# Kernel tuning notes

Measured on AMD Instinct MI355X. Metric: run time of the kernel, lower is better.

## Reference

```python
import jax, jax.numpy as jnp
from jax import lax
import numpy as np
from math import lgamma

N_MELS = 80; MEMORY_DIM = 512; PRENET = (256, 256)
ATTN_LSTM = 1024; ATTN_DIM = 128
N_STATIC = 8; SF = 21; N_DYN = 8; DF = 21
PRIOR_LEN = 11; ALPHA = 0.1; BETA = 0.9
DEC_LSTM = 1024; R = 2
B = 32; T_MELS = 800; T_ENC = 200


def _betabinom_pmf(k, n, a, b):
    lbeta = lambda x, y: lgamma(x) + lgamma(y) - lgamma(x + y)
    return np.exp(lgamma(n + 1) - lgamma(k + 1) - lgamma(n - k + 1) + lbeta(k + a, n - k + b) - lbeta(a, b))


def setup_inputs() -> dict:
    key = jax.random.key(0)
    ks = iter(jax.random.split(key, 40))
    w = lambda shape, s=0.05: jax.random.normal(next(ks), shape, jnp.float32) * s
    # prior filter, flipped as in the torch buffer (so cross-correlation == convolution with pmf)
    prior = np.array([_betabinom_pmf(k, PRIOR_LEN - 1, ALPHA, BETA) for k in range(PRIOR_LEN)], np.float32)[::-1].copy()
    return {
        "mels": w((B, N_MELS, T_MELS), 1.0),
        "memory": w((B, T_ENC, MEMORY_DIM), 1.0),
        "prenet_W1": w((PRENET[0], N_MELS)), "prenet_b1": jnp.zeros((PRENET[0],), jnp.float32),
        "prenet_W2": w((PRENET[1], PRENET[0])), "prenet_b2": jnp.zeros((PRENET[1],), jnp.float32),
        "attn_Wih": w((4 * ATTN_LSTM, PRENET[1] + MEMORY_DIM)), "attn_Whh": w((4 * ATTN_LSTM, ATTN_LSTM)),
        "attn_bih": jnp.zeros((4 * ATTN_LSTM,), jnp.float32), "attn_bhh": jnp.zeros((4 * ATTN_LSTM,), jnp.float32),
        "dca_Wq": w((ATTN_DIM, ATTN_LSTM)), "dca_bq": jnp.zeros((ATTN_DIM,), jnp.float32),
        "dca_V": w((N_DYN * DF, ATTN_DIM)),
        "dca_F": w((N_STATIC, 1, SF)),
        "dca_U": w((ATTN_DIM, N_STATIC)),
        "dca_T": w((ATTN_DIM, N_DYN)), "dca_Tb": jnp.zeros((ATTN_DIM,), jnp.float32),
        "dca_v": w((1, ATTN_DIM)),
        "prior": jnp.asarray(prior),
        "dec_Wih": w((4 * DEC_LSTM, ATTN_LSTM + MEMORY_DIM)), "dec_Whh": w((4 * DEC_LSTM, DEC_LSTM)),
        "dec_bih": jnp.zeros((4 * DEC_LSTM,), jnp.float32), "dec_bhh": jnp.zeros((4 * DEC_LSTM,), jnp.float32),
        "ac_W": w((N_MELS * R, DEC_LSTM + MEMORY_DIM)), "ac_b": jnp.zeros((N_MELS * R,), jnp.float32),
    }


def _lstm_cell(x, h, c, Wih, Whh, bih, bhh):
    g = x @ Wih.T + bih + h @ Whh.T + bhh
    i, f, gg, o = jnp.split(g, 4, axis=-1)  # torch gate order i,f,g,o
    c_new = jax.nn.sigmoid(f) * c + jax.nn.sigmoid(i) * jnp.tanh(gg)
    h_new = jax.nn.sigmoid(o) * jnp.tanh(c_new)
    return h_new, c_new


def _conv1d(x, k, pad, groups=1):
    # x: [B, Cin, T], k: [Cout, Cin/groups, K]; cross-correlation, like torch conv1d
    return lax.conv_general_dilated(x, k, (1,), [pad], feature_group_count=groups)


def _dca_step(query, memory, aw, prior, Wq, bq, V, Fk, U, Tw, Tb, v):
    Bsz, T = aw.shape
    # location prior: causal conv with (flipped) betabinom pmf
    p = _conv1d(aw[:, None, :], prior[None, None, :], (PRIOR_LEN - 1, 0))[:, 0, :]
    p = jnp.log(jnp.maximum(p, 1e-6))
    # dynamic filters predicted from query, applied per-batch via grouped conv
    G = jnp.tanh(query @ Wq.T + bq) @ V.T  # [B, N_DYN*DF]
    g = _conv1d(aw[None, :, :], G.reshape(Bsz * N_DYN, 1, DF), ((DF - 1) // 2, (DF - 1) // 2), groups=Bsz)
    g = g.reshape(Bsz, N_DYN, T).transpose(0, 2, 1)  # [B, T, N_DYN]
    # static location filters
    f = _conv1d(aw[:, None, :], Fk, ((SF - 1) // 2, (SF - 1) // 2)).transpose(0, 2, 1)  # [B, T, N_STATIC]
    e = (jnp.tanh(f @ U.T + g @ Tw.T + Tb) @ v.T)[:, :, 0] + p  # [B, T]
    aw_new = jax.nn.softmax(e, axis=-1)
    ctx = jnp.einsum("bt,btd->bd", aw_new, memory)
    return aw_new, ctx


def reference(mels, memory, prenet_W1, prenet_b1, prenet_W2, prenet_b2, attn_Wih, attn_Whh, attn_bih, attn_bhh, dca_Wq, dca_bq, dca_V, dca_F, dca_U, dca_T, dca_Tb, dca_v, prior, dec_Wih, dec_Whh, dec_bih, dec_bhh, ac_W, ac_b):
    Bsz, n_mels, T_mels = mels.shape
    T_enc = memory.shape[1]
    n_steps = T_mels // R
    go = jnp.zeros((Bsz, n_mels), mels.dtype)
    # teacher forcing: step t>0 consumes ground-truth frame at index t*R - 1
    tf = mels[:, :, R - 1::R][:, :, : n_steps - 1].transpose(2, 0, 1)
    frames = jnp.concatenate([go[None], tf], axis=0)  # [S, B, n_mels]
    aw0 = jnp.zeros((Bsz, T_enc), mels.dtype).at[:, 0].set(1.0)  # one-hot init attention
    carry0 = (jnp.zeros((Bsz, MEMORY_DIM), mels.dtype),
              jnp.zeros((Bsz, ATTN_LSTM), mels.dtype), jnp.zeros((Bsz, ATTN_LSTM), mels.dtype),
              jnp.zeros((Bsz, DEC_LSTM), mels.dtype), jnp.zeros((Bsz, DEC_LSTM), mels.dtype),
              aw0)

    def step(carry, frame):
        ctx, ah, acs, dh, dcs, aw = carry
        x = jax.nn.relu(frame @ prenet_W1.T + prenet_b1)
        x = jax.nn.relu(x @ prenet_W2.T + prenet_b2)
        ah, acs = _lstm_cell(jnp.concatenate([ctx, x], -1), ah, acs, attn_Wih, attn_Whh, attn_bih, attn_bhh)
        aw, ctx = _dca_step(ah, memory, aw, prior, dca_Wq, dca_bq, dca_V, dca_F, dca_U, dca_T, dca_Tb, dca_v)
        dh, dcs = _lstm_cell(jnp.concatenate([ah, ctx], -1), dh, dcs, dec_Wih, dec_Whh, dec_bih, dec_bhh)
        out = jnp.concatenate([dh, ctx], -1) @ ac_W.T + ac_b  # [B, n_mels*R]
        return (ctx, ah, acs, dh, dcs, aw), (out, aw)

    _, (outs, aws) = lax.scan(step, carry0, frames)
    # per-step [B, n_mels, R] frames concatenated along time (step-major)
    output_mels = outs.reshape(n_steps, Bsz, n_mels, R).transpose(1, 2, 0, 3).reshape(Bsz, n_mels, n_steps * R)
    alignments = aws.transpose(1, 2, 0)  # [B, T_enc, n_steps]
    return output_mels, alignments
```

## Files before the change

kernel.cpp:

```cpp
#include <hip/hip_runtime.h>
#include <hip/hip_bf16.h>

typedef unsigned short u16;
typedef unsigned int   u32;
typedef float f32x4 __attribute__((ext_vector_type(4)));

#define NTHR 256
#define NBLK 512
#define NGRP 64
#define GRPSZ 8
#define ROOT (NBLK - 1)

#define BATCH 32
#define TENC  200
#define NMELS 80
#define TMELS 800
#define NSTEP 400

#define BAR_CNT(g)  ((g)*32)
#define BAR_FLAG(g) (2048 + (g)*32)
#define BAR_GEN     4096

#define OFF_AHC   0
#define OFF_ACS   65536
#define OFF_DHC   98304
#define OFF_DCS   163840
#define OFF_CTX   196608
#define OFF_AW    229376
#define OFF_FBUF  236544
#define OFF_PBUF  287744
#define OFF_GPC   294912
#define OFF_X     425984
#define FLOAT_END 3702784
#define ZERO_CNT  236544

#define B_AWIH 0
#define B_AWHH 3145728
#define B_DWIH 7340032
#define B_DWHH 13631488
#define B_ACW  17825792
#define B_WQ   18071552
#define B_MEMT 18202624

#define NTLD4(dst, src) \
  asm volatile("global_load_dwordx4 %0, %1, off sc0 sc1" : "=v"(dst) : "v"(src))
#define NTLD1(dst, src) \
  asm volatile("global_load_dword %0, %1, off sc0 sc1" : "=v"(dst) : "v"(src))
#define NTFENCE() do { \
  asm volatile("s_waitcnt vmcnt(0)" ::: "memory"); \
  __builtin_amdgcn_sched_barrier(0); } while (0)

struct KArgs {
  const float *mels, *memory, *pW1, *pb1, *pW2, *pb2;
  const float *aWih, *aWhh, *abih, *abhh;
  const float *Wq, *bq, *V, *F, *U, *T, *Tb, *vv, *prior;
  const float *dWih, *dWhh, *dbih, *dbhh, *acW, *acb;
  float *out;
  float *ws;
  u16   *wb;
  int   *bar;
};

__device__ __forceinline__ float sigf(float x) {
  x = fminf(fmaxf(x, -30.f), 30.f);
  return 1.0f / (1.0f + __expf(-x));
}
__device__ __forceinline__ float ftanh(float x) {
  x = fminf(fmaxf(x, -15.f), 15.f);
  float e = __expf(2.f * x);
  return (e - 1.f) / (e + 1.f);
}
__device__ __forceinline__ float blo(u32 u) {
  union { u32 i; float f; } v; v.i = u << 16; return v.f;
}
__device__ __forceinline__ float bhi(u32 u) {
  union { u32 i; float f; } v; v.i = u & 0xffff0000u; return v.f;
}
__device__ __forceinline__ u16 f2b(float x) {
  __hip_bfloat16 h = __float2bfloat16(x);
  return *reinterpret_cast<u16*>(&h);
}

__device__ __forceinline__ void gbar(int* bar, int* s_bail, int& gen) {
  const int tid = threadIdx.x;
  const int bid = blockIdx.x;
  const int t = ++gen;
  __syncthreads();
  if (!*s_bail) {
    if (tid == 0) {
      int a_ = __hip_atomic_fetch_add(&bar[BAR_CNT(bid >> 3)], 1,
                                      __ATOMIC_RELEASE, __HIP_MEMORY_SCOPE_AGENT);
      if (a_ == GRPSZ - 1) {
        __hip_atomic_store(&bar[BAR_CNT(bid >> 3)], 0, __ATOMIC_RELAXED, __HIP_MEMORY_SCOPE_AGENT);
        __hip_atomic_store(&bar[BAR_FLAG(bid >> 3)], t, __ATOMIC_RELEASE, __HIP_MEMORY_SCOPE_AGENT);
      }
    }
    if (bid == ROOT) {
      if (tid < NGRP) {
        int it = 0;
        while (__hip_atomic_load(&bar[BAR_FLAG(tid)], __ATOMIC_RELAXED, __HIP_MEMORY_SCOPE_AGENT) < t) {
          __builtin_amdgcn_s_sleep(1);
          if (++it > (1 << 24)) { *s_bail = 1; break; }
        }
      }
      __syncthreads();
      if (tid == 0)
        __hip_atomic_store(&bar[BAR_GEN], t, __ATOMIC_RELEASE, __HIP_MEMORY_SCOPE_AGENT);
    } else if (tid == 0) {
      int it = 0;
      while (__hip_atomic_load(&bar[BAR_GEN], __ATOMIC_RELAXED, __HIP_MEMORY_SCOPE_AGENT) < t) {
        __builtin_amdgcn_s_sleep(1);
        if (++it > (1 << 24)) { *s_bail = 1; break; }
      }
    }
  }
  __syncthreads();
}

__device__ __forceinline__ float dotK(const float* xs, const u16* w, int K) {
  const uint4* wp = (const uint4*)w;
  const float4* xp = (const float4*)xs;
  float a0 = 0.f, a1 = 0.f, a2 = 0.f, a3 = 0.f;
  #pragma unroll 2
  for (int i = 0; i < (K >> 5); ++i) {
    uint4 w0 = wp[i*4+0], w1 = wp[i*4+1], w2 = wp[i*4+2], w3 = wp[i*4+3];
    float4 x0 = xp[i*8+0], x1 = xp[i*8+1], x2 = xp[i*8+2], x3 = xp[i*8+3];
    float4 x4 = xp[i*8+4], x5 = xp[i*8+5], x6 = xp[i*8+6], x7 = xp[i*8+7];
    a0 += blo(w0.x)*x0.x + bhi(w0.x)*x0.y + blo(w0.y)*x0.z + bhi(w0.y)*x0.w
        + blo(w0.z)*x1.x + bhi(w0.z)*x1.y + blo(w0.w)*x1.z + bhi(w0.w)*x1.w;
    a1 += blo(w1.x)*x2.x + bhi(w1.x)*x2.y + blo(w1.y)*x2.z + bhi(w1.y)*x2.w
        + blo(w1.z)*x3.x + bhi(w1.z)*x3.y + blo(w1.w)*x3.z + bhi(w1.w)*x3.w;
    a2 += blo(w2.x)*x4.x + bhi(w2.x)*x4.y + blo(w2.y)*x4.z + bhi(w2.y)*x4.w
        + blo(w2.z)*x5.x + bhi(w2.z)*x5.y + blo(w2.w)*x5.z + bhi(w2.w)*x5.w;
    a3 += blo(w3.x)*x6.x + bhi(w3.x)*x6.y + blo(w3.y)*x6.z + bhi(w3.y)*x6.w
        + blo(w3.z)*x7.x + bhi(w3.z)*x7.y + blo(w3.w)*x7.z + bhi(w3.w)*x7.w;
  }
  return (a0 + a1) + (a2 + a3);
}

__device__ __forceinline__ void j1_job(const KArgs& a, float* sm, int s) {
  const int tid = threadIdx.x, bid = blockIdx.x;
  const int ug = bid & 63, bg = bid >> 6;
  float* ws = a.ws;
  const u16* wb = a.wb;
  const int pprev = (s + 1) & 1, pcur = s & 1;
  const float* ctxp = ws + OFF_CTX + pprev * 16384;
  const float* ahp  = ws + OFF_AHC + pprev * 32768;
  const float* Xs   = ws + OFF_X + s * 8192;
  float* xbuf = sm;
  float* sred = sm + 8224;
  {
    const int bq = tid >> 6, lane = tid & 63;
    const int b = bg*4 + bq;
    const float* ctxb = ctxp + b*512;
    const float* Xb   = Xs + b*256;
    auto ap = [&](int idx) -> const f32x4* {
      if (idx < 128) return (const f32x4*)(ctxb + idx*4);
      if (idx < 192) return (const f32x4*)(Xb + (idx-128)*4);
      const int u = (idx-192)*4;
      return (const f32x4*)(ahp + (bg*64 + (u>>4))*64 + bq*16 + (u&15));
    };
    f32x4 v0,v1,v2,v3,v4,v5,v6;
    NTLD4(v0, ap(lane));       NTLD4(v1, ap(lane+64));
    NTLD4(v2, ap(lane+128));   NTLD4(v3, ap(lane+192));
    NTLD4(v4, ap(lane+256));   NTLD4(v5, ap(lane+320));
    NTLD4(v6, ap(lane+384));
    NTFENCE();
    f32x4* dst = (f32x4*)(xbuf + bq*1800);
    dst[lane] = v0; dst[lane+64] = v1; dst[lane+128] = v2; dst[lane+192] = v3;
    dst[lane+256] = v4; dst[lane+320] = v5; dst[lane+384] = v6;
  }
  __syncthreads();
  {
    const int r8 = tid >> 2, bsub = tid & 3;
    const int gate = r8 >> 4, ui = r8 & 15;
    const int rr = gate*1024 + ug*16 + ui;
    const float* xs = xbuf + bsub*1800;
    float acc = dotK(xs, wb + B_AWIH + rr*768, 768)
              + dotK(xs + 768, wb + B_AWHH + rr*1024, 1024)
              + a.abih[rr] + a.abhh[rr];
    sred[tid] = acc;
  }
  __syncthreads();
  if (tid < 64) {
    const int ui2 = tid >> 2, b2 = tid & 3;
    const float gi = sred[(ui2)*4 + b2];
    const float gf = sred[(16+ui2)*4 + b2];
    const float gg = sred[(32+ui2)*4 + b2];
    const float go = sred[(48+ui2)*4 + b2];
    float* acs = ws + OFF_ACS;
    const float c = sigf(gf)*acs[bid*64 + tid] + sigf(gi)*ftanh(gg);
    acs[bid*64 + tid] = c;
    (ws + OFF_AHC + pcur*32768)[bid*64 + b2*16 + ui2] = sigf(go)*ftanh(c);
  }
}

__device__ __forceinline__ void jg_job(const KArgs& a, float* sm, int s, int j) {
  const int tid = threadIdx.x;
  const int ug = j & 63, bg = j >> 6;
  float* ws = a.ws;
  const u16* wb = a.wb;
  const float* dhp = ws + OFF_DHC + ((s+1)&1)*32768;
  const float* ahp = ws + OFF_AHC + (s&1)*32768;
  float* xbuf = sm;
  __syncthreads();
  {
    const int bq = tid >> 6, lane = tid & 63;
    auto ap = [&](int idx) -> const f32x4* {
      if (idx < 256) { const int u = idx*4;
        return (const f32x4*)(dhp + (bg*64 + (u>>4))*64 + bq*16 + (u&15)); }
      const int u = (idx-256)*4;
      return (const f32x4*)(ahp + (bg*64 + (u>>4))*64 + bq*16 + (u&15));
    };
    f32x4 v0,v1,v2,v3,v4,v5,v6,v7;
    NTLD4(v0, ap(lane));       NTLD4(v1, ap(lane+64));
    NTLD4(v2, ap(lane+128));   NTLD4(v3, ap(lane+192));
    NTLD4(v4, ap(lane+256));   NTLD4(v5, ap(lane+320));
    NTLD4(v6, ap(lane+384));   NTLD4(v7, ap(lane+448));
    NTFENCE();
    f32x4* dst = (f32x4*)(xbuf + bq*2056);
    dst[lane] = v0; dst[lane+64] = v1; dst[lane+128] = v2; dst[lane+192] = v3;
    dst[lane+256] = v4; dst[lane+320] = v5; dst[lane+384] = v6; dst[lane+448] = v7;
  }
  __syncthreads();
  {
    const int r8 = tid >> 2, bsub = tid & 3;
    const int gate = r8 >> 4, ui = r8 & 15;
    const int rr = gate*1024 + ug*16 + ui;
    const float* xs = xbuf + bsub*2056;
    float acc = dotK(xs, wb + B_DWHH + rr*1024, 1024)
              + dotK(xs + 1024, wb + B_DWIH + rr*1536, 1024)
              + a.dbih[rr] + a.dbhh[rr];
    (ws + OFF_GPC)[j*256 + tid] = acc;
  }
}

__device__ __forceinline__ void p3_job(const KArgs& a, float* sm, int s) {
  const int tid = threadIdx.x, bid = blockIdx.x;
  const int ug = bid & 63, bg = bid >> 6;
  float* ws = a.ws;
  const u16* wb = a.wb;
  const float* ctxc = ws + OFF_CTX + (s&1)*16384;
  float* xbuf = sm;
  float* sred = sm + 8224;
  __syncthreads();
  const int bq = tid >> 6, lane = tid & 63;
  const int b = bg*4 + bq;
  f32x4 v0, v1; float gp;
  NTLD4(v0, (const f32x4*)(ctxc + b*512 + lane*4));
  NTLD4(v1, (const f32x4*)(ctxc + b*512 + (lane+64)*4));
  NTLD1(gp, (ws + OFF_GPC + bid*256 + tid));
  NTFENCE();
  ((f32x4*)(xbuf + bq*520))[lane] = v0;
  ((f32x4*)(xbuf + bq*520))[lane+64] = v1;
  __syncthreads();
  {
    const int r8 = tid >> 2, bsub = tid & 3;
    const int gate = r8 >> 4, ui = r8 & 15;
    const int rr = gate*1024 + ug*16 + ui;
    (void)gate; (void)ui;
    float acc = dotK(xbuf + bsub*520, wb + B_DWIH + rr*1536 + 1024, 512) + gp;
    sred[tid] = acc;
  }
  __syncthreads();
  if (tid < 64) {
    const int ui2 = tid >> 2, b2 = tid & 3;
    const float gi = sred[(ui2)*4 + b2];
    const float gf = sred[(16+ui2)*4 + b2];
    const float gg = sred[(32+ui2)*4 + b2];
    const float go = sred[(48+ui2)*4 + b2];
    float* dcs = ws + OFF_DCS;
    const float c = sigf(gf)*dcs[bid*64 + tid] + sigf(gi)*ftanh(gg);
    dcs[bid*64 + tid] = c;
    (ws + OFF_DHC + (s&1)*32768)[bid*64 + b2*16 + ui2] = sigf(go)*ftanh(c);
  }
}

__device__ __forceinline__ void j4_job(const KArgs& a, float* sm) {
  const int tid = threadIdx.x, b4 = blockIdx.x;
  float* ws = a.ws;
  float* aw   = ws + OFF_AW;
  float* fbuf = ws + OFF_FBUF;
  float* pbuf = ws + OFF_PBUF;
  __syncthreads();
  if (tid < 224) sm[tid] = (tid >= 10 && tid < 210) ? aw[b4*224 + tid - 10] : 0.f;
  __syncthreads();
  if (tid < 200) {
    #pragma unroll
    for (int j = 0; j < 8; ++j) {
      float p = 0.f;
      #pragma unroll
      for (int tau = 0; tau < 21; ++tau) p += sm[tid + tau] * a.F[j*21 + tau];
      fbuf[b4*1600 + tid*8 + j] = p;
    }
    float pp = 0.f;
    #pragma unroll
    for (int tau = 0; tau < 11; ++tau) pp += sm[tid + tau] * a.prior[tau];
    pbuf[b4*224 + tid] = __logf(fmaxf(pp, 1e-6f));
  }
}

__device__ __forceinline__ void outproj_job(const KArgs& a, float* sm, int sprev) {
  const int tid = threadIdx.x, bid = blockIdx.x;
  const int og = bid - 192, rg = og >> 3, bg = og & 7;
  const int pdm = sprev & 1;
  float* ws = a.ws;
  const u16* wb = a.wb;
  const float* dhp  = ws + OFF_DHC + pdm*32768;
  const float* ctxp = ws + OFF_CTX + pdm*16384;
  float* xbuf = sm;
  float* sred = sm + 8224;
  __syncthreads();
  {
    const int bq = tid >> 6, lane = tid & 63;
    const int b = bg*4 + bq;
    auto ap = [&](int idx) -> const f32x4* {
      if (idx < 256) { const int u = idx*4;
        return (const f32x4*)(dhp + (bg*64 + (u>>4))*64 + bq*16 + (u&15)); }
      return (const f32x4*)(ctxp + b*512 + (idx-256)*4);
    };
    f32x4 v0,v1,v2,v3,v4,v5;
    NTLD4(v0, ap(lane));       NTLD4(v1, ap(lane+64));
    NTLD4(v2, ap(lane+128));   NTLD4(v3, ap(lane+192));
    NTLD4(v4, ap(lane+256));   NTLD4(v5, ap(lane+320));
    NTFENCE();
    f32x4* dst = (f32x4*)(xbuf + bq*1544);
    dst[lane] = v0; dst[lane+64] = v1; dst[lane+128] = v2; dst[lane+192] = v3;
    dst[lane+256] = v4; dst[lane+320] = v5;
  }
  __syncthreads();
  {
    const int kc = tid & 7, r = (tid >> 3) & 7, bq = tid >> 6;
    const int rr = rg*8 + r;
    float p = dotK(xbuf + bq*1544 + kc*192, wb + B_ACW + rr*1536 + kc*192, 192);
    sred[tid] = p;
  }
  __syncthreads();
  if (tid < 32) {
    const int bq2 = tid >> 3, r2 = tid & 7;
    const int rr2 = rg*8 + r2, b2 = bg*4 + bq2;
    float tot = a.acb[rr2];
    #pragma unroll
    for (int q = 0; q < 8; ++q) tot += sred[bq2*64 + r2*8 + q];
    a.out[(b2*NMELS + (rr2 >> 1))*TMELS + sprev*2 + (rr2 & 1)] = tot;
  }
}

__device__ __forceinline__ void dca_step(const KArgs& a, float* sm, int s) {
  const int tid = threadIdx.x, b = blockIdx.x;
  const u16* wb = a.wb;
  float* ws = a.ws;
  const int pc = s & 1;
  const float* ahp = ws + OFF_AHC + pc*32768;
  float* ctx  = ws + OFF_CTX + pc*16384;
  float* aw   = ws + OFF_AW;
  const float* fbuf = ws + OFF_FBUF;
  const float* pbuf = ws + OFF_PBUF;
  float* s_ah  = sm;
  float* s_awp = sm + 1024;
  float* s_q   = sm + 1248;
  float* s_G   = sm + 1376;
  float* s_e   = sm + 1552;
  float* s_gg  = sm + 1760;
  float* s_ff  = sm + 3360;
  float* s_red = sm + 4960;
  float* s_awn = sm + 5216;
  f32x4 vah;
  {
    const int u = tid*4;
    NTLD4(vah, (const f32x4*)(ahp + ((b>>2)*64 + (u>>4))*64 + (b&3)*16 + (u&15)));
  }
  if (tid < 224) s_awp[tid] = (tid >= 10 && tid < 210) ? aw[b*224 + tid - 10] : 0.f;
  for (int i = tid; i < 1600; i += NTHR) s_ff[i] = fbuf[b*1600 + i];
  NTFENCE();
  *(f32x4*)(s_ah + tid*4) = vah;
  __syncthreads();
  {
    const int o = tid & 127, half = tid >> 7;
    const uint4* wq = (const uint4*)(wb + B_WQ + o*1024 + half*512);
    const float* xa = s_ah + half*512;
    float p = 0.f;
    #pragma unroll 8
    for (int q8 = 0; q8 < 64; ++q8) {
      uint4 w = wq[q8];
      const float* xq = xa + q8*8;
      p += blo(w.x)*xq[0] + bhi(w.x)*xq[1] + blo(w.y)*xq[2] + bhi(w.y)*xq[3]
         + blo(w.z)*xq[4] + bhi(w.z)*xq[5] + blo(w.w)*xq[6] + bhi(w.w)*xq[7];
    }
    s_red[tid] = p;
  }
  __syncthreads();
  if (tid < 128) s_q[tid] = ftanh(s_red[tid] + s_red[128 + tid] + a.bq[tid]);
  __syncthreads();
  if (tid < 168) {
    const float4* vp = (const float4*)(a.V + tid*128);
    float p = 0.f;
    #pragma unroll
    for (int q4 = 0; q4 < 32; ++q4) {
      float4 w = vp[q4];
      const float* xq = s_q + q4*4;
      p += w.x*xq[0] + w.y*xq[1] + w.z*xq[2] + w.w*xq[3];
    }
    s_G[tid] = p;
  }
  __syncthreads();
  for (int idx = tid; idx < 1600; idx += NTHR) {
    const int pos = idx >> 3, d = idx & 7;
    float p = 0.f;
    #pragma unroll
    for (int tau = 0; tau < 21; ++tau) p += s_awp[pos + tau] * s_G[d*21 + tau];
    s_gg[idx] = p;
  }
  __syncthreads();
  #pragma unroll 1
  for (int ro = 0; ro < 4; ++ro) {
    const int pos = ro*64 + (tid >> 2), sub = tid & 3;
    float av = 0.f;
    if (pos < 200) {
      const float* fpos = s_ff + pos*8;
      const float* gpos = s_gg + pos*8;
      #pragma unroll 4
      for (int fi = 0; fi < 32; ++fi) {
        const int ff = sub*32 + fi;
        const float4* Up = (const float4*)(a.U + ff*8);
        const float4* Tp = (const float4*)(a.T + ff*8);
        float4 u0 = Up[0], u1 = Up[1], t0 = Tp[0], t1 = Tp[1];
        float h = a.Tb[ff];
        h += u0.x*fpos[0] + u0.y*fpos[1] + u0.z*fpos[2] + u0.w*fpos[3]
           + u1.x*fpos[4] + u1.y*fpos[5] + u1.z*fpos[6] + u1.w*fpos[7];
        h += t0.x*gpos[0] + t0.y*gpos[1] + t0.z*gpos[2] + t0.w*gpos[3]
           + t1.x*gpos[4] + t1.y*gpos[5] + t1.z*gpos[6] + t1.w*gpos[7];
        av += a.vv[ff] * ftanh(h);
      }
    }
    av += __shfl_xor(av, 1);
    av += __shfl_xor(av, 2);
    if (sub == 0 && pos < 200) s_e[pos] = av + pbuf[b*224 + pos];
  }
  __syncthreads();
  float mval = (tid < 200) ? s_e[tid] : -1e30f;
  #pragma unroll
  for (int off = 32; off > 0; off >>= 1) mval = fmaxf(mval, __shfl_xor(mval, off));
  if ((tid & 63) == 0) s_red[tid >> 6] = mval;
  __syncthreads();
  const float m = fmaxf(fmaxf(s_red[0], s_red[1]), fmaxf(s_red[2], s_red[3]));
  const float ex = (tid < 200) ? __expf(s_e[tid] - m) : 0.f;
  float sv = ex;
  #pragma unroll
  for (int off = 32; off > 0; off >>= 1) sv += __shfl_xor(sv, off);
  if ((tid & 63) == 0) s_red[4 + (tid >> 6)] = sv;
  __syncthreads();
  const float inv = 1.f / (s_red[4] + s_red[5] + s_red[6] + s_red[7]);
  if (tid < 200) {
    const float awv = ex * inv;
    aw[b*224 + tid] = awv;
    s_awn[tid] = awv;
    a.out[2048000 + b*80000 + tid*400 + s] = awv;
  }
  __syncthreads();
  #pragma unroll 1
  for (int d = tid; d < 512; d += NTHR) {
    const uint4* mp = (const uint4*)(wb + B_MEMT + b*102400 + d*200);
    float p = 0.f;
    #pragma unroll 5
    for (int q = 0; q < 25; ++q) {
      uint4 v = mp[q];
      const float* aa = s_awn + q*8;
      p += blo(v.x)*aa[0] + bhi(v.x)*aa[1] + blo(v.y)*aa[2] + bhi(v.y)*aa[3]
         + blo(v.z)*aa[4] + bhi(v.z)*aa[5] + blo(v.w)*aa[6] + bhi(v.w)*aa[7];
    }
    ctx[b*512 + d] = p;
  }
}

__global__ __launch_bounds__(NTHR) void init_kernel(KArgs a) {
  const int gtid = blockIdx.x*NTHR + threadIdx.x;
  const int str = gridDim.x*NTHR;
  float* ws = a.ws;
  for (int i = gtid; i < 8192; i += str) a.bar[i] = 0;
  for (int i = gtid; i < ZERO_CNT; i += str) ws[i] = 0.f;
  float* aw = ws + OFF_AW;
  for (int i = gtid; i < 32*224; i += str) aw[i] = ((i % 224) == 0) ? 1.f : 0.f;
}

__global__ __launch_bounds__(NTHR) void conv_kernel(KArgs a) {
  const int gtid = blockIdx.x*NTHR + threadIdx.x;
  const int str = gridDim.x*NTHR;
  u16* wb = a.wb;
  for (int i = gtid; i < 3145728; i += str) wb[B_AWIH + i] = f2b(a.aWih[i]);
  for (int i = gtid; i < 4194304; i += str) wb[B_AWHH + i] = f2b(a.aWhh[i]);
  for (int i = gtid; i < 6291456; i += str) wb[B_DWIH + i] = f2b(a.dWih[i]);
  for (int i = gtid; i < 4194304; i += str) wb[B_DWHH + i] = f2b(a.dWhh[i]);
  for (int i = gtid; i < 245760;  i += str) wb[B_ACW  + i] = f2b(a.acW[i]);
  for (int i = gtid; i < 131072;  i += str) wb[B_WQ   + i] = f2b(a.Wq[i]);
  for (int i = gtid; i < 3276800; i += str) {
    const int b = i / 102400, rem = i - b*102400;
    const int d = rem / 200, t = rem - d*200;
    wb[B_MEMT + i] = f2b(a.memory[b*102400 + t*512 + d]);
  }
}

__global__ __launch_bounds__(NTHR) void prenet_kernel(KArgs a) {
  __shared__ float sm[384];
  const int tid = threadIdx.x;
  const int pair = blockIdx.x;
  const int s = pair >> 5, b = pair & 31;
  float* X = a.ws + OFF_X;
  if (tid < 80) {
    float v = 0.f;
    if (s > 0) v = a.mels[(b*NMELS + tid)*TMELS + 2*s - 1];
    sm[tid] = v;
  }
  __syncthreads();
  float a1 = a.pb1[tid];
  #pragma unroll 4
  for (int k = 0; k < 80; ++k) a1 += a.pW1[tid*80 + k] * sm[k];
  a1 = fmaxf(a1, 0.f);
  __syncthreads();
  sm[128 + tid] = a1;
  __syncthreads();
  float a2 = a.pb2[tid];
  #pragma unroll 4
  for (int k = 0; k < 256; ++k) a2 += a.pW2[tid*256 + k] * sm[128 + k];
  a2 = fmaxf(a2, 0.f);
  X[(s*BATCH + b)*256 + tid] = a2;
}

__global__ __launch_bounds__(NTHR, 2) void loop_kernel(KArgs a) {
  __shared__ float sm[8480];
  __shared__ int s_bail;
  const int tid = threadIdx.x;
  const int bid = blockIdx.x;
  int* bar = a.bar;
  int gen = 0;
  if (tid == 0) s_bail = 0;
  __syncthreads();

  j1_job(a, sm, 0);
  if (bid < 32) j4_job(a, sm);
  gbar(bar, &s_bail, gen);

  for (int s = 0; s < NSTEP; ++s) {
    if (bid < 32) {
      dca_step(a, sm, s);
    } else {
      jg_job(a, sm, s, bid - 32);
      if (bid < 64) jg_job(a, sm, s, bid + 448);
    }
    gbar(bar, &s_bail, gen);
    if (s + 1 < NSTEP) j1_job(a, sm, s + 1);
    p3_job(a, sm, s);
    if (bid < 32 && s + 1 < NSTEP) j4_job(a, sm);
    if (bid >= 192 && bid < 352 && s > 0) outproj_job(a, sm, s - 1);
    gbar(bar, &s_bail, gen);
  }

  if (bid >= 192 && bid < 352) outproj_job(a, sm, NSTEP - 1);
}

extern "C" void kernel_launch(void* const* d_in, const int* in_sizes, int n_in,
                              void* d_out, int out_size, void* d_ws, size_t ws_size,
                              hipStream_t stream) {
  (void)in_sizes; (void)n_in; (void)out_size; (void)ws_size;
  KArgs a;
  a.mels   = (const float*)d_in[0];
  a.memory = (const float*)d_in[1];
  a.pW1 = (const float*)d_in[2];  a.pb1 = (const float*)d_in[3];
  a.pW2 = (const float*)d_in[4];  a.pb2 = (const float*)d_in[5];
  a.aWih = (const float*)d_in[6]; a.aWhh = (const float*)d_in[7];
  a.abih = (const float*)d_in[8]; a.abhh = (const float*)d_in[9];
  a.Wq = (const float*)d_in[10];  a.bq = (const float*)d_in[11];
  a.V  = (const float*)d_in[12];  a.F  = (const float*)d_in[13];
  a.U  = (const float*)d_in[14];  a.T  = (const float*)d_in[15];
  a.Tb = (const float*)d_in[16];  a.vv = (const float*)d_in[17];
  a.prior = (const float*)d_in[18];
  a.dWih = (const float*)d_in[19]; a.dWhh = (const float*)d_in[20];
  a.dbih = (const float*)d_in[21]; a.dbhh = (const float*)d_in[22];
  a.acW  = (const float*)d_in[23]; a.acb  = (const float*)d_in[24];
  a.out = (float*)d_out;
  a.bar = (int*)d_ws;
  a.ws  = (float*)((char*)d_ws + 32768);
  a.wb  = (u16*)(a.ws + FLOAT_END);

  hipLaunchKernelGGL(init_kernel, dim3(512), dim3(NTHR), 0, stream, a);
  hipLaunchKernelGGL(conv_kernel, dim3(2048), dim3(NTHR), 0, stream, a);
  hipLaunchKernelGGL(prenet_kernel, dim3(NSTEP*BATCH), dim3(NTHR), 0, stream, a);
  hipLaunchKernelGGL(loop_kernel, dim3(NBLK), dim3(NTHR), 0, stream, a);
}
```

Before: 58.78 ms.

## Remap block-to-unit assignment, move outproj to first phase, use fast reciprocal

Remaps which unit group and batch group each block handles and adds a matching chunked layout (chunkW) for the hidden-state buffers. The output projection moves out of the second barrier phase into the first, running on blocks 64-223 alongside jg_job and the DCA step, which shortens the critical second phase. The prenet input X now uses a plain cached load. Divisions in sigmoid, tanh and softmax become hardware reciprocal approximations, and the outproj shared-memory staging is padded to reduce bank conflicts. The reciprocal approximation trades a small amount of accuracy for speed, and the new block mapping changes the data locality pattern.

```diff
diff --git a/kernel.cpp b/kernel.cpp
--- a/kernel.cpp
+++ b/kernel.cpp
@@ -61,14 +61,15 @@
   int   *bar;
 };
 
+__device__ __forceinline__ float frcp(float x) { return __builtin_amdgcn_rcpf(x); }
 __device__ __forceinline__ float sigf(float x) {
   x = fminf(fmaxf(x, -30.f), 30.f);
-  return 1.0f / (1.0f + __expf(-x));
+  return frcp(1.0f + __expf(-x));
 }
 __device__ __forceinline__ float ftanh(float x) {
   x = fminf(fmaxf(x, -15.f), 15.f);
   float e = __expf(2.f * x);
-  return (e - 1.f) / (e + 1.f);
+  return (e - 1.f) * frcp(e + 1.f);
 }
 __device__ __forceinline__ float blo(u32 u) {
   union { u32 i; float f; } v; v.i = u << 16; return v.f;
@@ -79,6 +80,9 @@
 __device__ __forceinline__ u16 f2b(float x) {
   __hip_bfloat16 h = __float2bfloat16(x);
   return *reinterpret_cast<u16*>(&h);
+}
+__device__ __forceinline__ int chunkW(int ug_, int bg_) {
+  return ((ug_ >> 3) + 8*bg_ + 64*(ug_ & 7)) * 64;
 }
 
 __device__ __forceinline__ void gbar(int* bar, int* s_bail, int& gen) {
@@ -140,7 +144,7 @@
 
 __device__ __forceinline__ void j1_job(const KArgs& a, float* sm, int s) {
   const int tid = threadIdx.x, bid = blockIdx.x;
-  const int ug = bid & 63, bg = bid >> 6;
+  const int ug = (bid & 7)*8 + (bid >> 6), bg = (bid >> 3) & 7;
   float* ws = a.ws;
   const u16* wb = a.wb;
   const int pprev = (s + 1) & 1, pcur = s & 1;
@@ -153,18 +157,16 @@
     const int bq = tid >> 6, lane = tid & 63;
     const int b = bg*4 + bq;
     const float* ctxb = ctxp + b*512;
-    const float* Xb   = Xs + b*256;
-    auto ap = [&](int idx) -> const f32x4* {
-      if (idx < 128) return (const f32x4*)(ctxb + idx*4);
-      if (idx < 192) return (const f32x4*)(Xb + (idx-128)*4);
-      const int u = (idx-192)*4;
-      return (const f32x4*)(ahp + (bg*64 + (u>>4))*64 + bq*16 + (u&15));
+    auto ah_at = [&](int idx) -> const f32x4* {
+      const int u = (idx - 192)*4;
+      return (const f32x4*)(ahp + chunkW(u >> 4, bg) + bq*16 + (u & 15));
     };
-    f32x4 v0,v1,v2,v3,v4,v5,v6;
-    NTLD4(v0, ap(lane));       NTLD4(v1, ap(lane+64));
-    NTLD4(v2, ap(lane+128));   NTLD4(v3, ap(lane+192));
-    NTLD4(v4, ap(lane+256));   NTLD4(v5, ap(lane+320));
-    NTLD4(v6, ap(lane+384));
+    f32x4 v0,v1,v3,v4,v5,v6;
+    NTLD4(v0, (const f32x4*)(ctxb + lane*4));
+    NTLD4(v1, (const f32x4*)(ctxb + (lane+64)*4));
+    NTLD4(v3, ah_at(lane+192)); NTLD4(v4, ah_at(lane+256));
+    NTLD4(v5, ah_at(lane+320)); NTLD4(v6, ah_at(lane+384));
+    f32x4 v2 = *((const f32x4*)(Xs + b*256 + lane*4));
     NTFENCE();
     f32x4* dst = (f32x4*)(xbuf + bq*1800);
     dst[lane] = v0; dst[lane+64] = v1; dst[lane+128] = v2; dst[lane+192] = v3;
@@ -197,7 +199,7 @@
 
 __device__ __forceinline__ void jg_job(const KArgs& a, float* sm, int s, int j) {
   const int tid = threadIdx.x;
-  const int ug = j & 63, bg = j >> 6;
+  const int ug = (j & 7)*8 + (j >> 6), bg = (j >> 3) & 7;
   float* ws = a.ws;
   const u16* wb = a.wb;
   const float* dhp = ws + OFF_DHC + ((s+1)&1)*32768;
@@ -208,9 +210,9 @@
     const int bq = tid >> 6, lane = tid & 63;
     auto ap = [&](int idx) -> const f32x4* {
       if (idx < 256) { const int u = idx*4;
-        return (const f32x4*)(dhp + (bg*64 + (u>>4))*64 + bq*16 + (u&15)); }
+        return (const f32x4*)(dhp + chunkW(u >> 4, bg) + bq*16 + (u & 15)); }
       const int u = (idx-256)*4;
-      return (const f32x4*)(ahp + (bg*64 + (u>>4))*64 + bq*16 + (u&15));
+      return (const f32x4*)(ahp + chunkW(u >> 4, bg) + bq*16 + (u & 15));
     };
     f32x4 v0,v1,v2,v3,v4,v5,v6,v7;
     NTLD4(v0, ap(lane));       NTLD4(v1, ap(lane+64));
@@ -237,7 +239,7 @@
 
 __device__ __forceinline__ void p3_job(const KArgs& a, float* sm, int s) {
   const int tid = threadIdx.x, bid = blockIdx.x;
-  const int ug = bid & 63, bg = bid >> 6;
+  const int ug = (bid & 7)*8 + (bid >> 6), bg = (bid >> 3) & 7;
   float* ws = a.ws;
   const u16* wb = a.wb;
   const float* ctxc = ws + OFF_CTX + (s&1)*16384;
@@ -258,7 +260,6 @@
     const int r8 = tid >> 2, bsub = tid & 3;
     const int gate = r8 >> 4, ui = r8 & 15;
     const int rr = gate*1024 + ug*16 + ui;
-    (void)gate; (void)ui;
     float acc = dotK(xbuf + bsub*520, wb + B_DWIH + rr*1536 + 1024, 512) + gp;
     sred[tid] = acc;
   }
@@ -302,7 +303,7 @@
 
 __device__ __forceinline__ void outproj_job(const KArgs& a, float* sm, int sprev) {
   const int tid = threadIdx.x, bid = blockIdx.x;
-  const int og = bid - 192, rg = og >> 3, bg = og & 7;
+  const int og = bid - 64, rg = og >> 3, bg = og & 7;
   const int pdm = sprev & 1;
   float* ws = a.ws;
   const u16* wb = a.wb;
@@ -316,7 +317,7 @@
     const int b = bg*4 + bq;
     auto ap = [&](int idx) -> const f32x4* {
       if (idx < 256) { const int u = idx*4;
-        return (const f32x4*)(dhp + (bg*64 + (u>>4))*64 + bq*16 + (u&15)); }
+        return (const f32x4*)(dhp + chunkW(u >> 4, bg) + bq*16 + (u & 15)); }
       return (const f32x4*)(ctxp + b*512 + (idx-256)*4);
     };
     f32x4 v0,v1,v2,v3,v4,v5;
@@ -324,15 +325,19 @@
     NTLD4(v2, ap(lane+128));   NTLD4(v3, ap(lane+192));
     NTLD4(v4, ap(lane+256));   NTLD4(v5, ap(lane+320));
     NTFENCE();
-    f32x4* dst = (f32x4*)(xbuf + bq*1544);
-    dst[lane] = v0; dst[lane+64] = v1; dst[lane+128] = v2; dst[lane+192] = v3;
-    dst[lane+256] = v4; dst[lane+320] = v5;
+    float* base = xbuf + bq*1600;
+    auto put = [&](int f, f32x4 v) {
+      const int cf = f / 48, wf = f % 48;
+      *(f32x4*)(base + cf*200 + wf*4) = v;
+    };
+    put(lane, v0); put(lane+64, v1); put(lane+128, v2);
+    put(lane+192, v3); put(lane+256, v4); put(lane+320, v5);
   }
   __syncthreads();
   {
     const int kc = tid & 7, r = (tid >> 3) & 7, bq = tid >> 6;
     const int rr = rg*8 + r;
-    float p = dotK(xbuf + bq*1544 + kc*192, wb + B_ACW + rr*1536 + kc*192, 192);
+    float p = dotK(xbuf + bq*1600 + kc*200, wb + B_ACW + rr*1536 + kc*192, 192);
     sred[tid] = p;
   }
   __syncthreads();
@@ -368,7 +373,7 @@
   f32x4 vah;
   {
     const int u = tid*4;
-    NTLD4(vah, (const f32x4*)(ahp + ((b>>2)*64 + (u>>4))*64 + (b&3)*16 + (u&15)));
+    NTLD4(vah, (const f32x4*)(ahp + chunkW(u >> 4, b >> 2) + (b & 3)*16 + (u & 15)));
   }
   if (tid < 224) s_awp[tid] = (tid >= 10 && tid < 210) ? aw[b*224 + tid - 10] : 0.f;
   for (int i = tid; i < 1600; i += NTHR) s_ff[i] = fbuf[b*1600 + i];
@@ -450,7 +455,7 @@
   for (int off = 32; off > 0; off >>= 1) sv += __shfl_xor(sv, off);
   if ((tid & 63) == 0) s_red[4 + (tid >> 6)] = sv;
   __syncthreads();
-  const float inv = 1.f / (s_red[4] + s_red[5] + s_red[6] + s_red[7]);
+  const float inv = frcp(s_red[4] + s_red[5] + s_red[6] + s_red[7]);
   if (tid < 200) {
     const float awv = ex * inv;
     aw[b*224 + tid] = awv;
@@ -546,16 +551,16 @@
     } else {
       jg_job(a, sm, s, bid - 32);
       if (bid < 64) jg_job(a, sm, s, bid + 448);
+      if (bid >= 64 && bid < 224 && s > 0) outproj_job(a, sm, s - 1);
     }
     gbar(bar, &s_bail, gen);
     if (s + 1 < NSTEP) j1_job(a, sm, s + 1);
     p3_job(a, sm, s);
     if (bid < 32 && s + 1 < NSTEP) j4_job(a, sm);
-    if (bid >= 192 && bid < 352 && s > 0) outproj_job(a, sm, s - 1);
     gbar(bar, &s_bail, gen);
   }
 
-  if (bid >= 192 && bid < 352) outproj_job(a, sm, NSTEP - 1);
+  if (bid >= 64 && bid < 224) outproj_job(a, sm, NSTEP - 1);
 }
 
 extern "C" void kernel_launch(void* const* d_in, const int* in_sizes, int n_in,
```

New measurement: 57.43 ms. 1.02x faster.
